# Kernel tuning notes

Hardware: AMD Instinct MI355X
Metric: run time of the kernel (lower is better)

The kernel has to match this reference:

```python
import jax, jax.numpy as jnp
import numpy as np

B, N, F_IN, F_OUT, T, K = 32, 512, 64, 64, 12, 3


def setup_inputs() -> dict:
    key = jax.random.key(0)
    k1, k2, k3, k4 = jax.random.split(key, 4)
    x = jax.random.normal(k1, (B, N, F_IN, T), dtype=jnp.float32)
    cheb_polys = jax.random.normal(k2, (K, N, N), dtype=jnp.float32)
    spatial_attention = jax.random.uniform(k3, (B, N, N), dtype=jnp.float32)
    Theta = jax.random.normal(k4, (K, F_IN, F_OUT), dtype=jnp.float32) * 0.1
    return {"x": x, "cheb_polys": cheb_polys, "spatial_attention": spatial_attention, "Theta": Theta}


def reference(x, cheb_polys, spatial_attention, Theta):
    # Original: out[b,n,o,t] = relu( sum_k ( (cheb[k]*att[b]).T @ x[b,:,:,t] ) @ Theta[k] )
    # i.e. out[b,n,o,t] = relu( sum_{k,m,f} cheb[k,m,n]*att[b,m,n]*x[b,m,f,t]*Theta[k,f,o] )
    # Fully vectorized over K and T; einsum picks an efficient contraction path
    # (att-premultiply then batched GEMMs), fusing the nested python loops.
    out = jnp.einsum(
        'kmn,bmn,bmft,kfo->bnot',
        cheb_polys, spatial_attention, x, Theta,
        optimize=True,
    )
    return jax.nn.relu(out)
```

## Files before the change

### kernel.cpp

```cpp
#include <hip/hip_runtime.h>

typedef __attribute__((ext_vector_type(4))) float f32x4;
typedef __attribute__((ext_vector_type(8))) short bf16x8;

typedef __attribute__((address_space(3))) unsigned char lds_b;
typedef const __attribute__((address_space(1))) unsigned char glb_b;

__device__ __forceinline__ void gload_lds16(const void* g, void* l) {
  __builtin_amdgcn_global_load_lds((glb_b*)g, (lds_b*)l, 16, 0, 0);
}

__device__ __forceinline__ unsigned short f2bf(float f) {
  union { float f; unsigned int u; } v; v.f = f;
  unsigned int r = v.u + 0x7fffu + ((v.u >> 16) & 1u);
  return (unsigned short)(r >> 16);
}

__global__ __launch_bounds__(256) void theta_prep_k(const float* __restrict__ Theta,
                                                    unsigned short* __restrict__ Tg) {
  const int tid = threadIdx.x;
#pragma unroll
  for (int j = 0; j < 12; ++j) {
    int i = tid + j * 256;
    int k = i >> 10, rr = i & 1023;
    int f = rr >> 4, o0 = (rr & 15) << 2;
    float4 v = *(const float4*)(Theta + ((size_t)(k * 64 + f)) * 64 + o0);
    float vv[4] = {v.x, v.y, v.z, v.w};
#pragma unroll
    for (int jj = 0; jj < 4; ++jj) {
      int o = o0 + jj;
      int byte = k * 8192 + o * 128 + ((((f >> 3) ^ (o & 7)) << 4) | ((f & 7) << 1));
      *(unsigned short*)((char*)Tg + byte) = f2bf(vv[jj]);
    }
  }
}

__global__ __launch_bounds__(256) void prep_fused_k(const float* __restrict__ x,
                                                    const float* __restrict__ cheb,
                                                    const float* __restrict__ att,
                                                    const unsigned short* __restrict__ Tg,
                                                    unsigned short* __restrict__ A_ws,
                                                    unsigned short* __restrict__ U_ws) {
  __shared__ __align__(16) char smem[24576];
  const int bid = blockIdx.x;
  const int tid = threadIdx.x;

  if (bid < 1024) {
    unsigned short* Xl = (unsigned short*)smem;
    const int b = bid >> 5, mt = bid & 31;
    const int m0 = mt * 16;
    const int lane = tid & 63, w = tid >> 6;
    const int c = lane & 15, q = lane >> 4;

    bf16x8 afr[3][2];
#pragma unroll
    for (int k = 0; k < 3; ++k)
#pragma unroll
      for (int h = 0; h < 2; ++h) {
        int g = h * 4 + q;
        afr[k][h] = *(const bf16x8*)((const char*)Tg +
                      k * 8192 + (w * 16 + c) * 128 + (((g ^ (c & 7)) << 4)));
      }

    const float* xb = x + ((size_t)(b * 512 + m0)) * 768;
#pragma unroll
    for (int j = 0; j < 12; ++j) {
      int i = tid + j * 256;
      int m = i / 192, r = i - m * 192;
      float4 v = *(const float4*)(xb + (size_t)m * 768 + r * 4);
      float vv[4] = {v.x, v.y, v.z, v.w};
#pragma unroll
      for (int jj = 0; jj < 4; ++jj) {
        int e = r * 4 + jj;
        int f = e / 12, t = e - f * 12;
        int byte = t * 2048 + m * 128 + ((((f >> 3) ^ (m & 7)) << 4) | ((f & 7) << 1));
        *(unsigned short*)((char*)Xl + byte) = f2bf(vv[jj]);
      }
    }
    __syncthreads();

    const int oc = (w * 16 + q * 4) * 192 + c;
    for (int t = 0; t < 12; ++t) {
      bf16x8 bfr[2];
#pragma unroll
      for (int h = 0; h < 2; ++h) {
        int g = h * 4 + q;
        bfr[h] = *(const bf16x8*)((char*)Xl + t * 2048 + c * 128 + (((g ^ (c & 7)) << 4)));
      }
#pragma unroll
      for (int k = 0; k < 3; ++k) {
        f32x4 acc = {0.f, 0.f, 0.f, 0.f};
        acc = __builtin_amdgcn_mfma_f32_16x16x32_bf16(afr[k][0], bfr[0], acc, 0, 0, 0);
        acc = __builtin_amdgcn_mfma_f32_16x16x32_bf16(afr[k][1], bfr[1], acc, 0, 0, 0);
        unsigned short* up = U_ws +
            ((size_t)((b * 3 + k) * 32 + mt)) * 12288 + t * 16 + oc;
#pragma unroll
        for (int r = 0; r < 4; ++r)
          up[r * 192] = f2bf(acc[r]);
      }
    }
  } else {
    float (*tile)[68] = (float(*)[68])smem;
    const int id = bid - 1024;
    const int m0 = (id & 7) * 64, n0 = ((id >> 3) & 7) * 64, b = id >> 6;
    const int rm = tid >> 2;
    const int c4 = tid & 3;
    for (int k = 0; k < 3; ++k) {
      const float* cp = cheb + ((size_t)(k * 512 + m0 + rm)) * 512 + n0 + c4 * 16;
      const float* ap = att  + ((size_t)(b * 512 + m0 + rm)) * 512 + n0 + c4 * 16;
#pragma unroll
      for (int j = 0; j < 4; ++j) {
        float4 cc = *(const float4*)(cp + j * 4);
        float4 aa = *(const float4*)(ap + j * 4);
        float4 p; p.x = cc.x * aa.x; p.y = cc.y * aa.y; p.z = cc.z * aa.z; p.w = cc.w * aa.w;
        *(float4*)&tile[rm][c4 * 16 + j * 4] = p;
      }
      __syncthreads();
      unsigned int pk[8];
#pragma unroll
      for (int i = 0; i < 8; ++i) {
        float v0 = tile[c4 * 16 + 2 * i][rm];
        float v1 = tile[c4 * 16 + 2 * i + 1][rm];
        pk[i] = (unsigned int)f2bf(v0) | ((unsigned int)f2bf(v1) << 16);
      }
      unsigned short* op = A_ws + ((size_t)(b * 512 + n0 + rm)) * 1536 + k * 512 + m0 + c4 * 16;
      uint4 w0; w0.x = pk[0]; w0.y = pk[1]; w0.z = pk[2]; w0.w = pk[3];
      uint4 w1; w1.x = pk[4]; w1.y = pk[5]; w1.z = pk[6]; w1.w = pk[7];
      ((uint4*)op)[0] = w0;
      ((uint4*)op)[1] = w1;
      __syncthreads();
    }
  }
}

__global__ __launch_bounds__(256) void gemm_k(const unsigned short* __restrict__ A_ws,
                                              const unsigned short* __restrict__ U_ws,
                                              float* __restrict__ out) {
  __shared__ unsigned short At[128 * 64];
  __shared__ unsigned short Bt[128 * 64];
  const int hw = blockIdx.x;
  const int logical = (hw & 7) * 96 + (hw >> 3);
  const int b = logical / 24;
  const int rem = logical - b * 24;
  const int nb = (rem / 6) * 128;
  const int otb = (rem % 6) * 128;

  const int tid = threadIdx.x;
  const int lane = tid & 63, w = tid >> 6;
  const int wr = w >> 1, wc = w & 1;
  const int q = lane >> 4;
  const int c = lane & 15;

  const int rl = lane >> 3;
  const int gsrc = (lane & 7) ^ rl;
  const int mi0 = (gsrc & 1) * 8;
  const int mtq = gsrc >> 1;
  f32x4 acc[4][4] = {};

  const int uOff = (otb + w * 8 + rl) * 16 + mi0;
  const unsigned short* aRow = A_ws + ((size_t)(b * 512 + nb + w * 8 + rl)) * 1536 + gsrc * 8;
  const int ldsRowBase = w * 8 * 64;

  for (int kt = 0; kt < 24; ++kt) {
    const int k = kt >> 3;
    const int mc = kt & 7;
    const unsigned short* uBase =
        U_ws + ((size_t)((b * 3 + k) * 32 + mc * 4 + mtq)) * 12288 + uOff;
#pragma unroll
    for (int i = 0; i < 4; ++i) {
      gload_lds16(aRow + (size_t)(i * 32) * 1536 + kt * 64, &At[ldsRowBase + i * 32 * 64]);
      gload_lds16(uBase + i * 512,                          &Bt[ldsRowBase + i * 32 * 64]);
    }
    __syncthreads();
#pragma unroll
    for (int h = 0; h < 2; ++h) {
      bf16x8 af[4], bfv[4];
#pragma unroll
      for (int mi = 0; mi < 4; ++mi) {
        int row = wr * 64 + mi * 16 + c;
        af[mi] = *(const bf16x8*)&At[row * 64 + (((h * 4 + q) ^ (row & 7)) << 3)];
      }
#pragma unroll
      for (int ni = 0; ni < 4; ++ni) {
        int row = wc * 64 + ni * 16 + c;
        bfv[ni] = *(const bf16x8*)&Bt[row * 64 + (((h * 4 + q) ^ (row & 7)) << 3)];
      }
#pragma unroll
      for (int mi = 0; mi < 4; ++mi)
#pragma unroll
        for (int ni = 0; ni < 4; ++ni)
          acc[mi][ni] = __builtin_amdgcn_mfma_f32_16x16x32_bf16(af[mi], bfv[ni], acc[mi][ni], 0, 0, 0);
    }
    __syncthreads();
  }
#pragma unroll
  for (int mi = 0; mi < 4; ++mi) {
#pragma unroll
    for (int r = 0; r < 4; ++r) {
      int n = nb + wr * 64 + mi * 16 + q * 4 + r;
      float* orow = out + ((size_t)(b * 512 + n)) * 768 + otb + wc * 64 + c;
#pragma unroll
      for (int ni = 0; ni < 4; ++ni)
        orow[ni * 16] = fmaxf(acc[mi][ni][r], 0.f);
    }
  }
}

__global__ __launch_bounds__(256) void fallback_k(const float* __restrict__ x,
                                                  const float* __restrict__ cheb,
                                                  const float* __restrict__ att,
                                                  const float* __restrict__ Theta,
                                                  float* __restrict__ out) {
  __shared__ float wsm[3][512];
  __shared__ float z[3][768];
  const int n = blockIdx.x, b = blockIdx.y;
  const int tid = threadIdx.x;
  for (int i = tid; i < 1536; i += 256) {
    int k = i >> 9, m = i & 511;
    wsm[k][m] = cheb[((size_t)(k * 512 + m)) * 512 + n] * att[((size_t)(b * 512 + m)) * 512 + n];
  }
  __syncthreads();
  float a0[3] = {0.f, 0.f, 0.f}, a1[3] = {0.f, 0.f, 0.f}, a2[3] = {0.f, 0.f, 0.f};
  const float* xb = x + (size_t)b * 512 * 768;
  for (int m = 0; m < 512; ++m) {
    float w0 = wsm[0][m], w1 = wsm[1][m], w2 = wsm[2][m];
    float x0 = xb[(size_t)m * 768 + tid];
    float x1 = xb[(size_t)m * 768 + tid + 256];
    float x2 = xb[(size_t)m * 768 + tid + 512];
    a0[0] += w0 * x0; a0[1] += w1 * x0; a0[2] += w2 * x0;
    a1[0] += w0 * x1; a1[1] += w1 * x1; a1[2] += w2 * x1;
    a2[0] += w0 * x2; a2[1] += w1 * x2; a2[2] += w2 * x2;
  }
#pragma unroll
  for (int k = 0; k < 3; ++k) {
    z[k][tid] = a0[k]; z[k][tid + 256] = a1[k]; z[k][tid + 512] = a2[k];
  }
  __syncthreads();
#pragma unroll
  for (int j = 0; j < 3; ++j) {
    int ot = tid + j * 256;
    int o = ot / 12, t = ot - o * 12;
    float s = 0.f;
    for (int k = 0; k < 3; ++k)
#pragma unroll
      for (int f = 0; f < 64; ++f)
        s += z[k][f * 12 + t] * Theta[((size_t)(k * 64 + f)) * 64 + o];
    out[((size_t)(b * 512 + n)) * 768 + ot] = fmaxf(s, 0.f);
  }
}

extern "C" void kernel_launch(void* const* d_in, const int* in_sizes, int n_in,
                              void* d_out, int out_size, void* d_ws, size_t ws_size,
                              hipStream_t stream) {
  const float* x     = (const float*)d_in[0];
  const float* cheb  = (const float*)d_in[1];
  const float* att   = (const float*)d_in[2];
  const float* Theta = (const float*)d_in[3];
  float* out = (float*)d_out;

  const size_t needA = (size_t)32 * 512 * 1536 * 2;
  const size_t needU = (size_t)32 * 3 * 768 * 512 * 2;
  const size_t needT = (size_t)3 * 64 * 64 * 2;

  if (ws_size >= needA + needU + needT) {
    unsigned short* A_ws = (unsigned short*)d_ws;
    unsigned short* U_ws = (unsigned short*)((char*)d_ws + needA);
    unsigned short* Tg   = (unsigned short*)((char*)d_ws + needA + needU);
    theta_prep_k<<<dim3(1), 256, 0, stream>>>(Theta, Tg);
    prep_fused_k<<<dim3(3072), 256, 0, stream>>>(x, cheb, att, Tg, A_ws, U_ws);
    gemm_k<<<dim3(768), 256, 0, stream>>>(A_ws, U_ws, out);
  } else {
    fallback_k<<<dim3(512, 32), 256, 0, stream>>>(x, cheb, att, Theta, out);
  }
}
```

Baseline: 102.8 us.

## Split U-projection blocks by time group and stage outputs in LDS for vector stores

The x·Theta projection part of the fused prep kernel now uses three times as many blocks, each handling a third of the 12 time steps. Results are staged through a padded LDS tile so each k slice is written to the workspace with 16-byte vector stores instead of scattered 2-byte stores. Smaller shared memory per block and more blocks aim to raise occupancy and parallelism, and the vector stores aim to improve global write coalescing. In exchange, every block still reads the full x tile and discards two thirds of it, which triples global reads of x, and two extra barriers per k are added.

```diff
diff --git a/kernel.cpp b/kernel.cpp
--- a/kernel.cpp
+++ b/kernel.cpp
@@ -41,16 +41,19 @@
                                                     const unsigned short* __restrict__ Tg,
                                                     unsigned short* __restrict__ A_ws,
                                                     unsigned short* __restrict__ U_ws) {
-  __shared__ __align__(16) char smem[24576];
+  __shared__ __align__(16) char smem[17408];
   const int bid = blockIdx.x;
   const int tid = threadIdx.x;
 
-  if (bid < 1024) {
+  if (bid < 3072) {
     unsigned short* Xl = (unsigned short*)smem;
-    const int b = bid >> 5, mt = bid & 31;
+    unsigned short* Uo = (unsigned short*)(smem + 8192);
+    const int tg = bid % 3, rest = bid / 3;
+    const int b = rest >> 5, mt = rest & 31;
     const int m0 = mt * 16;
     const int lane = tid & 63, w = tid >> 6;
     const int c = lane & 15, q = lane >> 4;
+    const int og = tid >> 3, sub = tid & 7;
 
     bf16x8 afr[3][2];
 #pragma unroll
@@ -67,41 +70,49 @@
     for (int j = 0; j < 12; ++j) {
       int i = tid + j * 256;
       int m = i / 192, r = i - m * 192;
+      int f = r / 3, tq = r - f * 3;
       float4 v = *(const float4*)(xb + (size_t)m * 768 + r * 4);
-      float vv[4] = {v.x, v.y, v.z, v.w};
-#pragma unroll
-      for (int jj = 0; jj < 4; ++jj) {
-        int e = r * 4 + jj;
-        int f = e / 12, t = e - f * 12;
-        int byte = t * 2048 + m * 128 + ((((f >> 3) ^ (m & 7)) << 4) | ((f & 7) << 1));
-        *(unsigned short*)((char*)Xl + byte) = f2bf(vv[jj]);
+      if (tq == tg) {
+        float vv[4] = {v.x, v.y, v.z, v.w};
+#pragma unroll
+        for (int jj = 0; jj < 4; ++jj) {
+          int byte = jj * 2048 + m * 128 + ((((f >> 3) ^ (m & 7)) << 4) | ((f & 7) << 1));
+          *(unsigned short*)((char*)Xl + byte) = f2bf(vv[jj]);
+        }
       }
     }
     __syncthreads();
 
-    const int oc = (w * 16 + q * 4) * 192 + c;
-    for (int t = 0; t < 12; ++t) {
-      bf16x8 bfr[2];
-#pragma unroll
-      for (int h = 0; h < 2; ++h) {
-        int g = h * 4 + q;
-        bfr[h] = *(const bf16x8*)((char*)Xl + t * 2048 + c * 128 + (((g ^ (c & 7)) << 4)));
-      }
-#pragma unroll
-      for (int k = 0; k < 3; ++k) {
-        f32x4 acc = {0.f, 0.f, 0.f, 0.f};
-        acc = __builtin_amdgcn_mfma_f32_16x16x32_bf16(afr[k][0], bfr[0], acc, 0, 0, 0);
-        acc = __builtin_amdgcn_mfma_f32_16x16x32_bf16(afr[k][1], bfr[1], acc, 0, 0, 0);
-        unsigned short* up = U_ws +
-            ((size_t)((b * 3 + k) * 32 + mt)) * 12288 + t * 16 + oc;
+    const size_t ureg = ((size_t)(b * 3) * 32 + mt) * 12288 + tg * 64;
+    for (int k = 0; k < 3; ++k) {
+      f32x4 acc[4];
+#pragma unroll
+      for (int tl = 0; tl < 4; ++tl) {
+        bf16x8 b0 = *(const bf16x8*)((char*)Xl + tl * 2048 + c * 128 + ((q ^ (c & 7)) << 4));
+        bf16x8 b1 = *(const bf16x8*)((char*)Xl + tl * 2048 + c * 128 + (((4 + q) ^ (c & 7)) << 4));
+        f32x4 a = {0.f, 0.f, 0.f, 0.f};
+        a = __builtin_amdgcn_mfma_f32_16x16x32_bf16(afr[k][0], b0, a, 0, 0, 0);
+        acc[tl] = __builtin_amdgcn_mfma_f32_16x16x32_bf16(afr[k][1], b1, acc[tl] = a, 0, 0, 0);
+      }
+      unsigned short* uo = Uo + (w * 16 + q * 4) * 68 + c;
+#pragma unroll
+      for (int tl = 0; tl < 4; ++tl)
 #pragma unroll
         for (int r = 0; r < 4; ++r)
-          up[r * 192] = f2bf(acc[r]);
-      }
+          uo[r * 68 + tl * 16] = f2bf(acc[tl][r]);
+      __syncthreads();
+      unsigned short* ub = U_ws + ureg + (size_t)k * 32 * 12288 + sub * 8;
+#pragma unroll
+      for (int ii = 0; ii < 2; ++ii) {
+        int o = ii * 32 + og;
+        bf16x8 v = *(const bf16x8*)(Uo + o * 68 + sub * 8);
+        *(bf16x8*)(ub + o * 192) = v;
+      }
+      __syncthreads();
     }
   } else {
     float (*tile)[68] = (float(*)[68])smem;
-    const int id = bid - 1024;
+    const int id = bid - 3072;
     const int m0 = (id & 7) * 64, n0 = ((id >> 3) & 7) * 64, b = id >> 6;
     const int rm = tid >> 2;
     const int c4 = tid & 3;
@@ -267,7 +278,7 @@
     unsigned short* U_ws = (unsigned short*)((char*)d_ws + needA);
     unsigned short* Tg   = (unsigned short*)((char*)d_ws + needA + needU);
     theta_prep_k<<<dim3(1), 256, 0, stream>>>(Theta, Tg);
-    prep_fused_k<<<dim3(3072), 256, 0, stream>>>(x, cheb, att, Tg, A_ws, U_ws);
+    prep_fused_k<<<dim3(5120), 256, 0, stream>>>(x, cheb, att, Tg, A_ws, U_ws);
     gemm_k<<<dim3(768), 256, 0, stream>>>(A_ws, U_ws, out);
   } else {
     fallback_k<<<dim3(512, 32), 256, 0, stream>>>(x, cheb, att, Theta, out);
```

Measured after the change: 109.6 us. +6.6%, slower.
